# Performance work log

Measured on AMD Instinct MI355X. Metric: run time of the kernel, lower is better.

The kernel has to match this reference:

```python
import jax, jax.numpy as jnp
import numpy as np

TEMPERATURE = 1.0

def setup_inputs() -> dict:
    key = jax.random.key(0)
    k1, k2 = jax.random.split(key)
    B, I, O = 256, 1024, 1024
    x = jax.random.normal(k1, (B, I), dtype=jnp.float32)
    # mimic TruncatedNormal(stddev=1/sqrt(input_size)) init
    w = jax.random.normal(k2, (I, O), dtype=jnp.float32) * (1.0 / np.sqrt(I))
    b = jnp.zeros((O,), dtype=jnp.float32)
    return {"x": x, "w": w, "b": b}

def reference(x, w, b):
    # z: [B, I, O] outer product per sample
    z = jnp.einsum('bi,io->bio', x, w)
    n = x.shape[-1]
    # per-output-neuron temperature softmax over the input dim I
    s = jax.nn.softmax(jnp.abs(z) / TEMPERATURE, axis=1)
    out = n * jnp.sum(z * s, axis=1)  # [B, O]
    return out + b
```

## Files before the change

### kernel.cpp

```cpp
#include <hip/hip_runtime.h>

#define BDIM 256
#define IDIM 1024
#define ODIM 1024

#define NW 8
#define TILE_OL 2
#define TILE_O (64 * TILE_OL)
#define TILE_B 4
#define QLEN (IDIM / NW)
#define CHUNK 8
#define NCHUNK (QLEN / CHUNK)

typedef float v2f __attribute__((ext_vector_type(2)));
typedef float v4f __attribute__((ext_vector_type(4)));

#if __has_builtin(__builtin_amdgcn_exp2f)
#define FAST_EXP2(v) __builtin_amdgcn_exp2f(v)
#else
#define FAST_EXP2(v) exp2f(v)
#endif

__global__ __launch_bounds__(512, 4)
void stl_kernel(const float* __restrict__ x,
                const float* __restrict__ w,
                const float* __restrict__ bias,
                float* __restrict__ out) {
  __shared__ float xs[TILE_B][IDIM];
  __shared__ float ps[NW][64][16];

  const int tx = threadIdx.x;
  const int ty = threadIdx.y;
  const int tid = ty * 64 + tx;
  const int o0 = blockIdx.x * TILE_O;
  const int b0 = blockIdx.y * TILE_B;

  const float LOG2E = 1.4426950408889634f;

#pragma unroll
  for (int k = 0; k < 2; ++k) {
    int f = tid + k * 512;
    int row = f >> 8;
    int col = f & 255;
    float4 v = ((const float4*)(x + (size_t)(b0 + row) * IDIM))[col];
    v.x *= LOG2E; v.y *= LOG2E; v.z *= LOG2E; v.w *= LOG2E;
    ((float4*)(&xs[row][0]))[col] = v;
  }
  __syncthreads();

  const int qbase = ty * QLEN;
  const float* wp = w + (size_t)qbase * ODIM + o0 + tx;

  const int rot = ty * 2;
#define CID(c) ((((c) + rot)) & (NCHUNK - 1))

  v2f an[TILE_OL][TILE_B], ad[TILE_OL][TILE_B];
#pragma unroll
  for (int s = 0; s < TILE_OL; ++s)
#pragma unroll
    for (int r = 0; r < TILE_B; ++r) { an[s][r] = (v2f){0.f, 0.f}; ad[s][r] = (v2f){0.f, 0.f}; }

  v2f wbuf[3][TILE_OL][CHUNK / 2];

#define WLOADI(bi, cc)                                                    \
  {                                                                       \
    const float* wq = wp + (size_t)((cc) * CHUNK) * ODIM;                 \
    _Pragma("unroll")                                                     \
    for (int u = 0; u < CHUNK / 2; ++u) {                                 \
      wbuf[bi][0][u].x = wq[(size_t)(2 * u) * ODIM];                      \
      wbuf[bi][0][u].y = wq[(size_t)(2 * u + 1) * ODIM];                  \
      wbuf[bi][1][u].x = wq[(size_t)(2 * u) * ODIM + 64];                 \
      wbuf[bi][1][u].y = wq[(size_t)(2 * u + 1) * ODIM + 64];             \
    }                                                                     \
  }

#define ROWPF(acc_n, acc_d, xpair, wpair)                                 \
  {                                                                       \
    v2f p = (xpair) * (wpair);                \
    v2f t;                                                                \
    t.x = FAST_EXP2(__builtin_fabsf(p.x));     \
    t.y = FAST_EXP2(__builtin_fabsf(p.y));                                \
    acc_n += p * t;                                         \
    acc_d += t;                                             \
  }

#define LOF(xq) __builtin_shufflevector(xq, xq, 0, 1)
#define HIF(xq) __builtin_shufflevector(xq, xq, 2, 3)

#define COMPUTEI(bi, cc)                                                  \
  {                                                                       \
    const int jb = qbase + (cc) * CHUNK;                                  \
    _Pragma("unroll")                                                     \
    for (int h = 0; h < 2; ++h) {                                         \
      v4f xq[TILE_B];                                                     \
      _Pragma("unroll")                                                   \
      for (int r = 0; r < TILE_B; ++r)                                    \
        xq[r] = *(const v4f*)(&xs[r][jb + h * 4]);                        \
      _Pragma("unroll")                                                   \
      for (int r = 0; r < TILE_B; ++r) {                                  \
        ROWPF(an[0][r], ad[0][r], LOF(xq[r]), wbuf[bi][0][h * 2])         \
        ROWPF(an[0][r], ad[0][r], HIF(xq[r]), wbuf[bi][0][h * 2 + 1])     \
        ROWPF(an[1][r], ad[1][r], LOF(xq[r]), wbuf[bi][1][h * 2])         \
        ROWPF(an[1][r], ad[1][r], HIF(xq[r]), wbuf[bi][1][h * 2 + 1])     \
      }                                                                   \
    }                                                                     \
  }

  WLOADI(0, CID(0))
  WLOADI(1, CID(1))
#pragma unroll
  for (int c = 0; c < NCHUNK; ++c) {
    if (c + 2 < NCHUNK) WLOADI((c + 2) % 3, CID(c + 2))
    COMPUTEI(c % 3, CID(c))
  }

#pragma unroll
  for (int s = 0; s < TILE_OL; ++s) {
    *(float4*)(&ps[ty][tx][s * 8 + 0]) =
        make_float4(an[s][0].x + an[s][0].y, an[s][1].x + an[s][1].y,
                    an[s][2].x + an[s][2].y, an[s][3].x + an[s][3].y);
    *(float4*)(&ps[ty][tx][s * 8 + 4]) =
        make_float4(ad[s][0].x + ad[s][0].y, ad[s][1].x + ad[s][1].y,
                    ad[s][2].x + ad[s][2].y, ad[s][3].x + ad[s][3].y);
  }
  __syncthreads();

  if (ty == 0) {
    const float LN2 = 0.6931471805599453f;
    const float scale = (float)IDIM * LN2;
#pragma unroll
    for (int s = 0; s < TILE_OL; ++s) {
      float n[4] = {0, 0, 0, 0}, d[4] = {0, 0, 0, 0};
#pragma unroll
      for (int q = 0; q < NW; ++q) {
        float4 a = *(const float4*)(&ps[q][tx][s * 8 + 0]);
        float4 b2 = *(const float4*)(&ps[q][tx][s * 8 + 4]);
        n[0] += a.x; n[1] += a.y; n[2] += a.z; n[3] += a.w;
        d[0] += b2.x; d[1] += b2.y; d[2] += b2.z; d[3] += b2.w;
      }
      const int o = o0 + tx + s * 64;
      const float bo = bias[o];
#pragma unroll
      for (int r = 0; r < 4; ++r)
        out[(size_t)(b0 + r) * ODIM + o] = scale * n[r] / d[r] + bo;
    }
  }
}

extern "C" void kernel_launch(void* const* d_in, const int* in_sizes, int n_in,
                              void* d_out, int out_size, void* d_ws, size_t ws_size,
                              hipStream_t stream) {
  const float* x = (const float*)d_in[0];
  const float* w = (const float*)d_in[1];
  const float* b = (const float*)d_in[2];
  float* out = (float*)d_out;

  dim3 grid(ODIM / TILE_O, BDIM / TILE_B);
  dim3 block(64, NW);
  stl_kernel<<<grid, block, 0, stream>>>(x, w, b, out);
}
```

Baseline: 92.38 us.

## Halve batch tile, raise occupancy, use double-buffered weight loads and spread final reduction

Cuts the batch tile from 4 to 2 rows per block and raises the launch-bounds occupancy target from 4 to 6, shrinking per-thread accumulators and shared memory. This is meant to let more waves run per CU to hide latency. The triple-buffered, fully unrolled, per-wave-rotated weight prefetch becomes a rolled ping-pong double buffer without rotation, and the final cross-wave reduction now runs on 256 threads instead of one wave. In exchange, each weight element loaded from memory is reused across half as many batch rows, so weight traffic per unit of work doubles. Removing the chunk rotation may also increase bank conflicts in shared memory.

```diff
diff --git a/kernel.cpp b/kernel.cpp
--- a/kernel.cpp
+++ b/kernel.cpp
@@ -7,7 +7,7 @@
 #define NW 8
 #define TILE_OL 2
 #define TILE_O (64 * TILE_OL)
-#define TILE_B 4
+#define TILE_B 2
 #define QLEN (IDIM / NW)
 #define CHUNK 8
 #define NCHUNK (QLEN / CHUNK)
@@ -21,13 +21,13 @@
 #define FAST_EXP2(v) exp2f(v)
 #endif
 
-__global__ __launch_bounds__(512, 4)
+__global__ __launch_bounds__(512, 6)
 void stl_kernel(const float* __restrict__ x,
                 const float* __restrict__ w,
                 const float* __restrict__ bias,
                 float* __restrict__ out) {
   __shared__ float xs[TILE_B][IDIM];
-  __shared__ float ps[NW][64][16];
+  __shared__ float ps[NW][64][8];
 
   const int tx = threadIdx.x;
   const int ty = threadIdx.y;
@@ -37,11 +37,9 @@
 
   const float LOG2E = 1.4426950408889634f;
 
-#pragma unroll
-  for (int k = 0; k < 2; ++k) {
-    int f = tid + k * 512;
-    int row = f >> 8;
-    int col = f & 255;
+  {
+    int row = tid >> 8;
+    int col = tid & 255;
     float4 v = ((const float4*)(x + (size_t)(b0 + row) * IDIM))[col];
     v.x *= LOG2E; v.y *= LOG2E; v.z *= LOG2E; v.w *= LOG2E;
     ((float4*)(&xs[row][0]))[col] = v;
@@ -51,26 +49,23 @@
   const int qbase = ty * QLEN;
   const float* wp = w + (size_t)qbase * ODIM + o0 + tx;
 
-  const int rot = ty * 2;
-#define CID(c) ((((c) + rot)) & (NCHUNK - 1))
-
   v2f an[TILE_OL][TILE_B], ad[TILE_OL][TILE_B];
 #pragma unroll
   for (int s = 0; s < TILE_OL; ++s)
 #pragma unroll
     for (int r = 0; r < TILE_B; ++r) { an[s][r] = (v2f){0.f, 0.f}; ad[s][r] = (v2f){0.f, 0.f}; }
 
-  v2f wbuf[3][TILE_OL][CHUNK / 2];
+  v2f wA0[CHUNK / 2], wA1[CHUNK / 2], wB0[CHUNK / 2], wB1[CHUNK / 2];
 
-#define WLOADI(bi, cc)                                                    \
+#define WLOADF(d0_, d1_, cc)                                              \
   {                                                                       \
     const float* wq = wp + (size_t)((cc) * CHUNK) * ODIM;                 \
     _Pragma("unroll")                                                     \
     for (int u = 0; u < CHUNK / 2; ++u) {                                 \
-      wbuf[bi][0][u].x = wq[(size_t)(2 * u) * ODIM];                      \
-      wbuf[bi][0][u].y = wq[(size_t)(2 * u + 1) * ODIM];                  \
-      wbuf[bi][1][u].x = wq[(size_t)(2 * u) * ODIM + 64];                 \
-      wbuf[bi][1][u].y = wq[(size_t)(2 * u + 1) * ODIM + 64];             \
+      d0_[u].x = wq[(size_t)(2 * u) * ODIM];                              \
+      d0_[u].y = wq[(size_t)(2 * u + 1) * ODIM];                          \
+      d1_[u].x = wq[(size_t)(2 * u) * ODIM + 64];                         \
+      d1_[u].y = wq[(size_t)(2 * u + 1) * ODIM + 64];                     \
     }                                                                     \
   }
 
@@ -87,7 +82,7 @@
 #define LOF(xq) __builtin_shufflevector(xq, xq, 0, 1)
 #define HIF(xq) __builtin_shufflevector(xq, xq, 2, 3)
 
-#define COMPUTEI(bi, cc)                                                  \
+#define COMPUTEF(wc0, wc1, cc)                                            \
   {                                                                       \
     const int jb = qbase + (cc) * CHUNK;                                  \
     _Pragma("unroll")                                                     \
@@ -98,52 +93,44 @@
         xq[r] = *(const v4f*)(&xs[r][jb + h * 4]);                        \
       _Pragma("unroll")                                                   \
       for (int r = 0; r < TILE_B; ++r) {                                  \
-        ROWPF(an[0][r], ad[0][r], LOF(xq[r]), wbuf[bi][0][h * 2])         \
-        ROWPF(an[0][r], ad[0][r], HIF(xq[r]), wbuf[bi][0][h * 2 + 1])     \
-        ROWPF(an[1][r], ad[1][r], LOF(xq[r]), wbuf[bi][1][h * 2])         \
-        ROWPF(an[1][r], ad[1][r], HIF(xq[r]), wbuf[bi][1][h * 2 + 1])     \
+        ROWPF(an[0][r], ad[0][r], LOF(xq[r]), wc0[h * 2])                 \
+        ROWPF(an[0][r], ad[0][r], HIF(xq[r]), wc0[h * 2 + 1])             \
+        ROWPF(an[1][r], ad[1][r], LOF(xq[r]), wc1[h * 2])                 \
+        ROWPF(an[1][r], ad[1][r], HIF(xq[r]), wc1[h * 2 + 1])             \
       }                                                                   \
     }                                                                     \
   }
 
-  WLOADI(0, CID(0))
-  WLOADI(1, CID(1))
-#pragma unroll
-  for (int c = 0; c < NCHUNK; ++c) {
-    if (c + 2 < NCHUNK) WLOADI((c + 2) % 3, CID(c + 2))
-    COMPUTEI(c % 3, CID(c))
+  WLOADF(wA0, wA1, 0)
+  for (int c = 0; c < NCHUNK; c += 2) {
+    WLOADF(wB0, wB1, c + 1)
+    COMPUTEF(wA0, wA1, c)
+    WLOADF(wA0, wA1, (c + 2) & (NCHUNK - 1))
+    COMPUTEF(wB0, wB1, c + 1)
   }
 
-#pragma unroll
-  for (int s = 0; s < TILE_OL; ++s) {
-    *(float4*)(&ps[ty][tx][s * 8 + 0]) =
-        make_float4(an[s][0].x + an[s][0].y, an[s][1].x + an[s][1].y,
-                    an[s][2].x + an[s][2].y, an[s][3].x + an[s][3].y);
-    *(float4*)(&ps[ty][tx][s * 8 + 4]) =
-        make_float4(ad[s][0].x + ad[s][0].y, ad[s][1].x + ad[s][1].y,
-                    ad[s][2].x + ad[s][2].y, ad[s][3].x + ad[s][3].y);
-  }
+  *(float4*)(&ps[ty][tx][0]) =
+      make_float4(an[0][0].x + an[0][0].y, an[0][1].x + an[0][1].y,
+                  an[1][0].x + an[1][0].y, an[1][1].x + an[1][1].y);
+  *(float4*)(&ps[ty][tx][4]) =
+      make_float4(ad[0][0].x + ad[0][0].y, ad[0][1].x + ad[0][1].y,
+                  ad[1][0].x + ad[1][0].y, ad[1][1].x + ad[1][1].y);
   __syncthreads();
 
-  if (ty == 0) {
+  if (tid < 256) {
+    const int txp = tid & 63;
+    const int s = (tid >> 6) & 1;
+    const int bq = tid >> 7;
+    float n = 0.f, d = 0.f;
+#pragma unroll
+    for (int wv = 0; wv < NW; ++wv) {
+      n += ps[wv][txp][s * 2 + bq];
+      d += ps[wv][txp][4 + s * 2 + bq];
+    }
     const float LN2 = 0.6931471805599453f;
     const float scale = (float)IDIM * LN2;
-#pragma unroll
-    for (int s = 0; s < TILE_OL; ++s) {
-      float n[4] = {0, 0, 0, 0}, d[4] = {0, 0, 0, 0};
-#pragma unroll
-      for (int q = 0; q < NW; ++q) {
-        float4 a = *(const float4*)(&ps[q][tx][s * 8 + 0]);
-        float4 b2 = *(const float4*)(&ps[q][tx][s * 8 + 4]);
-        n[0] += a.x; n[1] += a.y; n[2] += a.z; n[3] += a.w;
-        d[0] += b2.x; d[1] += b2.y; d[2] += b2.z; d[3] += b2.w;
-      }
-      const int o = o0 + tx + s * 64;
-      const float bo = bias[o];
-#pragma unroll
-      for (int r = 0; r < 4; ++r)
-        out[(size_t)(b0 + r) * ODIM + o] = scale * n[r] / d[r] + bo;
-    }
+    const int o = o0 + s * 64 + txp;
+    out[(size_t)(b0 + bq) * ODIM + o] = scale * n / d + bias[o];
   }
 }
 
```

After: 94.67 us. 1.02x slower.
